# Kernel tuning notes

Hardware: AMD Instinct MI355X
Metric: run time of the kernel (lower is better)

Reference implementation:

```python
import jax, jax.numpy as jnp
import numpy as np

# ---- problem constants (mirror AdjustInstanceArea __init__ args) ----
NUM_NODES = 2_000_000
NUM_MOVABLE = 1_500_000
NUM_FILLER = 400_000
NUM_NETS = 1_500_000
PINS_PER_NET = 4                       # uniform netpin_start = arange(0, P+1, 4)
NUM_PINS = NUM_NETS * PINS_PER_NET
XL, XH, YL, YH = 0.0, 1000.0, 0.0, 1000.0
NBX = NBY = 512
BIN_W = (XH - XL) / NBX
BIN_H = (YH - YL) / NBY
UNIT_H_CAP = 1.5                       # unit horizontal routing capacity
UNIT_V_CAP = 1.5                       # unit vertical routing capacity
MAX_RATE = 2.0                         # max_route_opt_adjust_rate
MIN_RATE = 1.0 / MAX_RATE
EPS = 1e-6


def setup_inputs() -> dict:
    key = jax.random.key(0)
    k = jax.random.split(key, 4)
    x = jax.random.uniform(k[0], (NUM_NODES,), jnp.float32, XL, XH - 4.0)
    y = jax.random.uniform(k[1], (NUM_NODES,), jnp.float32, YL, YH - 4.0)
    pos = jnp.concatenate([x, y])                      # [2*num_nodes], x then y

    # pins clustered around net centers (realistic small net bboxes)
    rng = np.random.default_rng(0)
    centers = rng.uniform(0.0, 1000.0, size=(NUM_NETS, 1, 2)).astype(np.float32)
    jit = rng.uniform(-20.0, 20.0, size=(NUM_NETS, PINS_PER_NET, 2)).astype(np.float32)
    ppos = np.clip(centers + jit, 0.0, 1000.0)         # [nets, pins_per_net, 2], in net order

    # flat_netpin: pin ids grouped by net; pin_pos indexed by pin id
    flat_netpin = rng.permutation(NUM_PINS).astype(np.int32)
    px = np.empty(NUM_PINS, np.float32); py = np.empty(NUM_PINS, np.float32)
    px[flat_netpin] = ppos[..., 0].reshape(-1)
    py[flat_netpin] = ppos[..., 1].reshape(-1)
    pin_pos = jnp.concatenate([jnp.asarray(px), jnp.asarray(py)])  # [2*num_pins]

    pin2net = jnp.asarray(np.repeat(np.arange(NUM_NETS, dtype=np.int32), PINS_PER_NET))

    node_size_x = jax.random.uniform(k[2], (NUM_NODES,), jnp.float32, 1.0, 4.0)
    node_size_y = jax.random.uniform(k[3], (NUM_NODES,), jnp.float32, 1.0, 4.0)
    return {"pos": pos, "pin_pos": pin_pos,
            "node_size_x": node_size_x, "node_size_y": node_size_y,
            "flat_netpin": jnp.asarray(flat_netpin), "pin2net": pin2net}


def _rect_accum(vals, blx, bly, bhx, bhy):
    """Accumulate vals over inclusive bin rectangles via difference map + 2D cumsum."""
    D = jnp.zeros((NBX + 1, NBY + 1), vals.dtype)
    D = D.at[blx, bly].add(vals)
    D = D.at[bhx + 1, bly].add(-vals)
    D = D.at[blx, bhy + 1].add(-vals)
    D = D.at[bhx + 1, bhy + 1].add(vals)
    return jnp.cumsum(jnp.cumsum(D, axis=0), axis=1)[:NBX, :NBY]


def reference(pos, pin_pos, node_size_x, node_size_y, flat_netpin, pin2net):
    # ---- InstanceRouteOptimizationArea: RUDY routing demand per bin ----
    px = pin_pos[:NUM_PINS][flat_netpin].reshape(NUM_NETS, PINS_PER_NET)
    py = pin_pos[NUM_PINS:][flat_netpin].reshape(NUM_NETS, PINS_PER_NET)
    net_xl = jnp.min(px, axis=1); net_xh = jnp.max(px, axis=1)
    net_yl = jnp.min(py, axis=1); net_yh = jnp.max(py, axis=1)
    bw = net_xh - net_xl
    bh = net_yh - net_yl
    barea = jnp.maximum(bw * bh, EPS)
    dens_h = bw / barea                                # horizontal wire density
    dens_v = bh / barea                                # vertical wire density

    blx = jnp.clip(jnp.floor((net_xl - XL) / BIN_W), 0, NBX - 1).astype(jnp.int32)
    bhx = jnp.clip(jnp.floor((net_xh - XL) / BIN_W), 0, NBX - 1).astype(jnp.int32)
    bly = jnp.clip(jnp.floor((net_yl - YL) / BIN_H), 0, NBY - 1).astype(jnp.int32)
    bhy = jnp.clip(jnp.floor((net_yh - YL) / BIN_H), 0, NBY - 1).astype(jnp.int32)

    util_h = _rect_accum(dens_h, blx, bly, bhx, bhy) / UNIT_H_CAP
    util_v = _rect_accum(dens_v, blx, bly, bhx, bhy) / UNIT_V_CAP

    # per-movable-node utilization (gather at node center bin)
    x = pos[:NUM_NODES]; y = pos[NUM_NODES:]
    nsx_m = node_size_x[:NUM_MOVABLE]; nsy_m = node_size_y[:NUM_MOVABLE]
    cx = x[:NUM_MOVABLE] + 0.5 * nsx_m
    cy = y[:NUM_MOVABLE] + 0.5 * nsy_m
    bix = jnp.clip(jnp.floor((cx - XL) / BIN_W), 0, NBX - 1).astype(jnp.int32)
    biy = jnp.clip(jnp.floor((cy - YL) / BIN_H), 0, NBY - 1).astype(jnp.int32)
    util = jnp.maximum(util_h[bix, biy], util_v[bix, biy])
    ratio = jnp.clip(util, MIN_RATE, MAX_RATE)

    area_old = nsx_m * nsy_m
    instance_route_area = area_old * ratio

    # ---- AdjustInstanceArea: rescale under max_total_area budget ----
    filler_area_old = jnp.sum(node_size_x[NUM_NODES - NUM_FILLER:] *
                              node_size_y[NUM_NODES - NUM_FILLER:])
    max_total_area = jnp.sum(area_old) + filler_area_old
    scale = jnp.minimum(1.0, max_total_area / jnp.maximum(jnp.sum(instance_route_area), EPS))
    new_area = instance_route_area * scale
    sr = jnp.sqrt(new_area / jnp.maximum(area_old, EPS))
    nsx_new = nsx_m * sr
    nsy_new = nsy_m * sr

    # keep cell centers fixed while resizing
    x_out = x.at[:NUM_MOVABLE].add(0.5 * (nsx_m - nsx_new))
    y_out = y.at[:NUM_MOVABLE].add(0.5 * (nsy_m - nsy_new))

    # fillers absorb leftover area budget
    fscale = jnp.sqrt(jnp.maximum(max_total_area - jnp.sum(new_area), 0.0) /
                      jnp.maximum(filler_area_old, EPS))
    nsx_out = node_size_x.at[:NUM_MOVABLE].set(nsx_new)
    nsx_out = nsx_out.at[NUM_NODES - NUM_FILLER:].multiply(fscale)
    nsy_out = node_size_y.at[:NUM_MOVABLE].set(nsy_new)
    nsy_out = nsy_out.at[NUM_NODES - NUM_FILLER:].multiply(fscale)

    return jnp.concatenate([x_out, y_out, nsx_out, nsy_out])  # [4*num_nodes]
```

## Files before the change

### kernel.cpp

```cpp
#include <hip/hip_runtime.h>
#include <hip/hip_fp16.h>
#include <math.h>

#define N_NODES   2000000
#define N_MOVABLE 1500000
#define N_FILLER  400000
#define N_NETS    1500000
#define N_PINS    (N_NETS * 4)
#define NB        512
#define NT        16
#define TILE      32
#define NBUCKET   (NT * NT)
#define CAP       10240
#define NSLICE    4
#define NMAPS     NSLICE
#define RED_BLOCKS 1024

#define NQ        24
#define QRNG      250000
#define NXCD      8
#define RPX       3
#define PIN_PER_XCD (QRNG * RPX)
#define P2CHUNK   4096
#define P2CHUNKS  ((PIN_PER_XCD + P2CHUNK - 1) / P2CHUNK)

#define SB_SHIFT  14
#define SB_CAP    16384
#define NSB       ((N_PINS + SB_CAP - 1) / SB_CAP)

__device__ __forceinline__ int bin_idx(float v) {
    float b = floorf(v / 1.953125f);
    b = fminf(fmaxf(b, 0.0f), 511.0f);
    return (int)b;
}

__global__ __launch_bounds__(1024)
void p1_bucketq_kernel(const int* __restrict__ fnp,
                       uint2* __restrict__ qslab,
                       unsigned* __restrict__ g_qptr) {
    __shared__ unsigned hist[NQ];
    __shared__ unsigned hbase[NQ];
    int t = threadIdx.x;
    if (t < NQ) hist[t] = 0;
    __syncthreads();

    int s0 = blockIdx.x * 4096 + t * 4;
    unsigned q[4]; unsigned qb[4]; unsigned rk[4]; bool val[4];
    if (s0 + 3 < N_PINS) {
        int4 f = *reinterpret_cast<const int4*>(fnp + s0);
        q[0] = (unsigned)f.x; q[1] = (unsigned)f.y;
        q[2] = (unsigned)f.z; q[3] = (unsigned)f.w;
        val[0] = val[1] = val[2] = val[3] = true;
    } else {
        #pragma unroll
        for (int j = 0; j < 4; ++j) {
            val[j] = (s0 + j < N_PINS);
            q[j] = val[j] ? (unsigned)fnp[s0 + j] : 0u;
        }
    }
    #pragma unroll
    for (int j = 0; j < 4; ++j) {
        qb[j] = q[j] / (unsigned)QRNG;
        rk[j] = val[j] ? atomicAdd(&hist[qb[j]], 1u) : 0u;
    }
    __syncthreads();
    if (t < NQ) {
        unsigned c = hist[t];
        hbase[t] = c ? atomicAdd(&g_qptr[t], c) : 0u;
    }
    __syncthreads();
    #pragma unroll
    for (int j = 0; j < 4; ++j) {
        if (val[j]) {
            unsigned idx = qb[j] * (unsigned)QRNG + hbase[qb[j]] + rk[j];
            qslab[idx] = make_uint2(q[j], (unsigned)(s0 + j));
        }
    }
}

__global__ __launch_bounds__(1024)
void p2_gather_kernel(const uint2* __restrict__ qslab,
                      const float* __restrict__ pin_pos,
                      uint2* __restrict__ sslab,
                      unsigned* __restrict__ xcd_ctr,
                      unsigned* __restrict__ g_sptr) {
    __shared__ unsigned hist[NSB];
    __shared__ unsigned hbase[NSB];
    __shared__ unsigned sh_c;
    int k = blockIdx.x & (NXCD - 1);
    int t = threadIdx.x;

    for (;;) {
        if (t == 0) sh_c = atomicAdd(&xcd_ctr[k], 1u);
        __syncthreads();
        unsigned c = sh_c;
        __syncthreads();
        if (c >= (unsigned)P2CHUNKS) break;

        for (int i = t; i < NSB; i += 1024) hist[i] = 0;
        __syncthreads();

        uint2 rec[4]; int sb[4]; unsigned rk[4]; bool val[4];
        #pragma unroll
        for (int j = 0; j < 4; ++j) {
            unsigned s = c * P2CHUNK + t + j * 1024;
            val[j] = (s < (unsigned)PIN_PER_XCD);
            sb[j] = 0; rk[j] = 0;
            if (val[j]) {
                unsigned rl = s / (unsigned)QRNG;
                unsigned ridx = s - rl * (unsigned)QRNG;
                unsigned r = (unsigned)k + 8u * rl;
                uint2 qr = qslab[r * (unsigned)QRNG + ridx];
                float x = pin_pos[qr.x];
                float y = pin_pos[qr.x + N_PINS];
                unsigned xq = __float2uint_rn(x * 64.0f);
                unsigned yq = __float2uint_rn(y * 64.0f);
                rec[j] = make_uint2(qr.y, xq | (yq << 16));
                sb[j] = (int)(qr.y >> SB_SHIFT);
                rk[j] = atomicAdd(&hist[sb[j]], 1u);
            }
        }
        __syncthreads();
        for (int i = t; i < NSB; i += 1024) {
            unsigned h = hist[i];
            hbase[i] = h ? atomicAdd(&g_sptr[i], h) : 0u;
        }
        __syncthreads();
        #pragma unroll
        for (int j = 0; j < 4; ++j) {
            if (val[j]) sslab[(size_t)sb[j] * SB_CAP + hbase[sb[j]] + rk[j]] = rec[j];
        }
        __syncthreads();
    }
}

__device__ __forceinline__ uint2 pack_tile_rec(float bw, float bh,
                                               unsigned blx, unsigned bhx,
                                               unsigned bly, unsigned bhy,
                                               int* tb) {
    float barea = fmaxf(bw * bh, 1e-6f);
    float vh = fminf((bw / barea) * (1.0f / 1.5f), 60000.0f);
    float vv = fminf((bh / barea) * (1.0f / 1.5f), 60000.0f);
    *tb = (int)((bly >> 5) * NT + (blx >> 5));
    __half2 h = __float22half2_rn(make_float2(vh, vv));
    uint2 r;
    r.x = *reinterpret_cast<unsigned*>(&h);
    r.y = blx | (bly << 9) | ((bhx + 1 - blx) << 18) | ((bhy + 1 - bly) << 23);
    return r;
}

__global__ __launch_bounds__(512)
void p3_netred_kernel(const uint2* __restrict__ sslab,
                      uint2* __restrict__ tslab,
                      unsigned* __restrict__ g_tptr) {
    __shared__ unsigned mnx[4096], mxx[4096], mny[4096], mxy[4096];
    __shared__ unsigned hist[NBUCKET];
    __shared__ unsigned hbase[NBUCKET];
    int bid = blockIdx.x, t = threadIdx.x;
    int base_slot = bid * SB_CAP;
    int cnt  = min(SB_CAP, N_PINS - base_slot);
    int base_net = bid * (SB_CAP / 4);
    int nets = min(SB_CAP / 4, N_NETS - base_net);

    for (int i = t; i < 4096; i += 512) {
        mnx[i] = 0xFFFFFFFFu; mny[i] = 0xFFFFFFFFu; mxx[i] = 0u; mxy[i] = 0u;
    }
    for (int i = t; i < NBUCKET; i += 512) hist[i] = 0;
    __syncthreads();

    for (int i = t; i < cnt; i += 512) {
        uint2 rc = sslab[(size_t)base_slot + i];
        unsigned nl = (rc.x >> 2) - (unsigned)base_net;
        unsigned xq = rc.y & 0xFFFFu, yq = rc.y >> 16;
        atomicMin(&mnx[nl], xq); atomicMax(&mxx[nl], xq);
        atomicMin(&mny[nl], yq); atomicMax(&mxy[nl], yq);
    }
    __syncthreads();

    uint2 rec[8]; int tb[8]; unsigned rk[8];
    #pragma unroll
    for (int u = 0; u < 8; ++u) {
        int j = t + u * 512;
        tb[u] = -1;
        if (j < nets) {
            unsigned xl = mnx[j], xh = mxx[j], yl = mny[j], yh = mxy[j];
            float bw = (float)(xh - xl) * 0.015625f;
            float bh = (float)(yh - yl) * 0.015625f;
            unsigned blx = min(xl / 125u, 511u), bhx = min(xh / 125u, 511u);
            unsigned bly = min(yl / 125u, 511u), bhy = min(yh / 125u, 511u);
            rec[u] = pack_tile_rec(bw, bh, blx, bhx, bly, bhy, &tb[u]);
            rk[u] = atomicAdd(&hist[tb[u]], 1u);
        }
    }
    __syncthreads();
    if (t < NBUCKET) {
        unsigned h = hist[t];
        hbase[t] = h ? atomicAdd(&g_tptr[t], h) : 0u;
    }
    __syncthreads();
    #pragma unroll
    for (int u = 0; u < 8; ++u) {
        if (tb[u] >= 0) tslab[(size_t)tb[u] * CAP + hbase[tb[u]] + rk[u]] = rec[u];
    }
}

__global__ void pack_kernel(const float* __restrict__ pin_pos,
                            float2* __restrict__ pp) {
    int i = blockIdx.x * blockDim.x + threadIdx.x;
    if (i >= N_PINS / 4) return;
    float4 a = reinterpret_cast<const float4*>(pin_pos)[i];
    float4 b = reinterpret_cast<const float4*>(pin_pos + N_PINS)[i];
    float4* o = reinterpret_cast<float4*>(pp + 4 * (size_t)i);
    o[0] = make_float4(a.x, b.x, a.y, b.y);
    o[1] = make_float4(a.z, b.z, a.w, b.w);
}

template <bool PACKED>
__device__ __forceinline__ uint2 make_rec_f(const float* __restrict__ pin_pos,
                                            const float2* __restrict__ pp,
                                            int4 fp, int* tb) {
    float2 p0, p1, p2, p3;
    if (PACKED) {
        p0 = pp[fp.x]; p1 = pp[fp.y]; p2 = pp[fp.z]; p3 = pp[fp.w];
    } else {
        p0 = make_float2(pin_pos[fp.x], pin_pos[N_PINS + fp.x]);
        p1 = make_float2(pin_pos[fp.y], pin_pos[N_PINS + fp.y]);
        p2 = make_float2(pin_pos[fp.z], pin_pos[N_PINS + fp.z]);
        p3 = make_float2(pin_pos[fp.w], pin_pos[N_PINS + fp.w]);
    }
    float xl = fminf(fminf(p0.x, p1.x), fminf(p2.x, p3.x));
    float xh = fmaxf(fmaxf(p0.x, p1.x), fmaxf(p2.x, p3.x));
    float yl = fminf(fminf(p0.y, p1.y), fminf(p2.y, p3.y));
    float yh = fmaxf(fmaxf(p0.y, p1.y), fmaxf(p2.y, p3.y));
    unsigned blx = bin_idx(xl), bhx = bin_idx(xh);
    unsigned bly = bin_idx(yl), bhy = bin_idx(yh);
    return pack_tile_rec(xh - xl, yh - yl, blx, bhx, bly, bhy, tb);
}

template <bool PACKED>
__global__ __launch_bounds__(1024)
void gather_bin_kernel(const float* __restrict__ pin_pos,
                       const float2* __restrict__ pp,
                       const int* __restrict__ fnp,
                       uint2* __restrict__ slab,
                       unsigned* __restrict__ g_ptr) {
    __shared__ unsigned hist[NBUCKET];
    __shared__ unsigned hbase[NBUCKET];
    int t = threadIdx.x;
    if (t < NBUCKET) hist[t] = 0;
    __syncthreads();

    int n0 = blockIdx.x * 4096 + t;
    bool v[4]; int4 fp[4]; uint2 r[4]; int b[4]; unsigned rk[4];
    #pragma unroll
    for (int k = 0; k < 4; ++k) {
        int n = n0 + k * 1024;
        v[k] = (n < N_NETS);
        fp[k] = v[k] ? *reinterpret_cast<const int4*>(fnp + 4 * (size_t)n)
                     : make_int4(0, 0, 0, 0);
    }
    #pragma unroll
    for (int k = 0; k < 4; ++k) {
        b[k] = 0;
        if (v[k]) r[k] = make_rec_f<PACKED>(pin_pos, pp, fp[k], &b[k]);
    }
    #pragma unroll
    for (int k = 0; k < 4; ++k) rk[k] = v[k] ? atomicAdd(&hist[b[k]], 1u) : 0u;
    __syncthreads();
    if (t < NBUCKET) {
        unsigned c = hist[t];
        hbase[t] = c ? atomicAdd(&g_ptr[t], c) : 0u;
    }
    __syncthreads();
    #pragma unroll
    for (int k = 0; k < 4; ++k) {
        if (v[k]) {
            unsigned s = hbase[b[k]] + rk[k];
            if (s < CAP) slab[(size_t)b[k] * CAP + s] = r[k];
        }
    }
}

__device__ __forceinline__ void rec_process(uint2 r, int x0, int y0,
                                            float2* acc) {
    float2 v = __half22float2(*reinterpret_cast<const __half2*>(&r.x));
    unsigned g = r.y;
    int ax0 = (int)(g & 511u);
    int ay0 = (int)((g >> 9) & 511u);
    int ax1 = ax0 + (int)((g >> 18) & 31u);
    int ay1 = ay0 + (int)((g >> 23) & 31u);
    int X0 = ax0 - x0, Y0 = ay0 - y0;
    int X1 = ax1 - x0, Y1 = ay1 - y0;
    bool iX0 = (unsigned)X0 < TILE, iX1 = (unsigned)X1 < TILE;
    bool iY0 = (unsigned)Y0 < TILE, iY1 = (unsigned)Y1 < TILE;
    if (iX0 && iY0) { atomicAdd(&acc[X0 * TILE + Y0].x,  v.x); atomicAdd(&acc[X0 * TILE + Y0].y,  v.y); }
    if (iX1 && iY0) { atomicAdd(&acc[X1 * TILE + Y0].x, -v.x); atomicAdd(&acc[X1 * TILE + Y0].y, -v.y); }
    if (iX0 && iY1) { atomicAdd(&acc[X0 * TILE + Y1].x, -v.x); atomicAdd(&acc[X0 * TILE + Y1].y, -v.y); }
    if (iX1 && iY1) { atomicAdd(&acc[X1 * TILE + Y1].x,  v.x); atomicAdd(&acc[X1 * TILE + Y1].y,  v.y); }
}

__global__ __launch_bounds__(256)
void accum_kernel(const uint2* __restrict__ slab,
                  const unsigned* __restrict__ g_cnt,
                  float2* __restrict__ Dp) {
    __shared__ float2 acc[TILE * TILE];
    int wg = blockIdx.x;
    int sl = wg & (NSLICE - 1), tile = wg >> 2;
    int tx = tile & (NT - 1), ty = tile >> 4;
    int tid = threadIdx.x;

    for (int i = tid; i < TILE * TILE; i += 256) acc[i] = make_float2(0.f, 0.f);
    __syncthreads();

    int x0 = tx * TILE, y0 = ty * TILE;
    #pragma unroll
    for (int dy = -1; dy <= 0; ++dy) {
        int sy = ty + dy; if (sy < 0) continue;
        #pragma unroll
        for (int dx = -1; dx <= 0; ++dx) {
            int sx = tx + dx; if (sx < 0) continue;
            int sb = sy * NT + sx;
            unsigned cnt = min(g_cnt[sb], (unsigned)CAP);
            unsigned lo = (cnt * (unsigned)sl) >> 2;
            unsigned hi = (cnt * (unsigned)(sl + 1)) >> 2;
            const uint2* recs = slab + (size_t)sb * CAP;
            unsigned i = lo + tid;
            for (; i + 768 < hi; i += 1024) {
                uint2 r0 = recs[i];
                uint2 r1 = recs[i + 256];
                uint2 r2 = recs[i + 512];
                uint2 r3 = recs[i + 768];
                rec_process(r0, x0, y0, acc);
                rec_process(r1, x0, y0, acc);
                rec_process(r2, x0, y0, acc);
                rec_process(r3, x0, y0, acc);
            }
            for (; i < hi; i += 256) rec_process(recs[i], x0, y0, acc);
        }
    }
    __syncthreads();

    float2* D = Dp + (size_t)sl * NB * NB;
    for (int i = tid; i < TILE * TILE; i += 256) {
        int X = i >> 5, Y = i & 31;
        D[(size_t)(x0 + X) * NB + (y0 + Y)] = acc[i];
    }
}

__global__ __launch_bounds__(512)
void scanA_kernel(const float2* __restrict__ Dp, float2* __restrict__ S) {
    __shared__ float2 s[NB];
    int x = blockIdx.x, t = threadIdx.x;
    float2 a = make_float2(0.f, 0.f);
    #pragma unroll
    for (int m = 0; m < NMAPS; ++m) {
        float2 v = Dp[(size_t)m * NB * NB + (size_t)x * NB + t];
        a.x += v.x; a.y += v.y;
    }
    s[t] = a;
    __syncthreads();
    for (int off = 1; off < NB; off <<= 1) {
        float2 u = s[t];
        if (t >= off) { float2 w = s[t - off]; u.x += w.x; u.y += w.y; }
        __syncthreads();
        s[t] = u;
        __syncthreads();
    }
    S[(size_t)x * NB + t] = s[t];
}

__global__ __launch_bounds__(512)
void scanB_kernel(float2* __restrict__ S) {
    __shared__ float2 s[NB];
    int y = blockIdx.x, t = threadIdx.x;
    s[t] = S[(size_t)t * NB + y];
    __syncthreads();
    for (int off = 1; off < NB; off <<= 1) {
        float2 u = s[t];
        if (t >= off) { float2 w = s[t - off]; u.x += w.x; u.y += w.y; }
        __syncthreads();
        s[t] = u;
        __syncthreads();
    }
    S[(size_t)t * NB + y] = s[t];
}

__global__ __launch_bounds__(256)
void reduce_kernel(const float* __restrict__ pos,
                   const float* __restrict__ nsx,
                   const float* __restrict__ nsy,
                   const float2* __restrict__ S,
                   double* __restrict__ partials) {
    const int MQ = N_MOVABLE / 4;
    const int TQ = MQ + N_FILLER / 4;
    double a_old = 0.0, a_route = 0.0, a_fill = 0.0;
    int stride = gridDim.x * blockDim.x;
    for (int q = blockIdx.x * blockDim.x + threadIdx.x; q < TQ; q += stride) {
        if (q < MQ) {
            int i = 4 * q;
            float4 x4  = *reinterpret_cast<const float4*>(pos + i);
            float4 y4  = *reinterpret_cast<const float4*>(pos + N_NODES + i);
            float4 sx4 = *reinterpret_cast<const float4*>(nsx + i);
            float4 sy4 = *reinterpret_cast<const float4*>(nsy + i);
            float xs[4] = {x4.x, x4.y, x4.z, x4.w};
            float ys[4] = {y4.x, y4.y, y4.z, y4.w};
            float sxs[4] = {sx4.x, sx4.y, sx4.z, sx4.w};
            float sys[4] = {sy4.x, sy4.y, sy4.z, sy4.w};
            #pragma unroll
            for (int k = 0; k < 4; ++k) {
                int bx = bin_idx(xs[k] + 0.5f * sxs[k]);
                int by = bin_idx(ys[k] + 0.5f * sys[k]);
                float2 u2 = S[(size_t)bx * NB + by];
                float ratio = fminf(fmaxf(fmaxf(u2.x, u2.y), 0.5f), 2.0f);
                float area = sxs[k] * sys[k];
                a_old += (double)area;
                a_route += (double)(area * ratio);
            }
        } else {
            int j = (N_NODES - N_FILLER) + 4 * (q - MQ);
            float4 sx4 = *reinterpret_cast<const float4*>(nsx + j);
            float4 sy4 = *reinterpret_cast<const float4*>(nsy + j);
            a_fill += (double)(sx4.x * sy4.x + sx4.y * sy4.y +
                               sx4.z * sy4.z + sx4.w * sy4.w);
        }
    }
    for (int off = 32; off > 0; off >>= 1) {
        a_old   += __shfl_down(a_old, off);
        a_route += __shfl_down(a_route, off);
        a_fill  += __shfl_down(a_fill, off);
    }
    __shared__ double sd[4][3];
    int wid = threadIdx.x >> 6, lane = threadIdx.x & 63;
    if (lane == 0) { sd[wid][0] = a_old; sd[wid][1] = a_route; sd[wid][2] = a_fill; }
    __syncthreads();
    if (threadIdx.x == 0) {
        double s0 = 0, s1 = 0, s2 = 0;
        for (int w = 0; w < 4; ++w) { s0 += sd[w][0]; s1 += sd[w][1]; s2 += sd[w][2]; }
        partials[blockIdx.x * 3 + 0] = s0;
        partials[blockIdx.x * 3 + 1] = s1;
        partials[blockIdx.x * 3 + 2] = s2;
    }
}

__global__ __launch_bounds__(256)
void finish_kernel(const double* __restrict__ partials,
                   double* __restrict__ sums) {
    int t = threadIdx.x;
    double s0 = 0, s1 = 0, s2 = 0;
    for (int r = t; r < RED_BLOCKS; r += 256) {
        s0 += partials[r * 3 + 0];
        s1 += partials[r * 3 + 1];
        s2 += partials[r * 3 + 2];
    }
    for (int off = 32; off > 0; off >>= 1) {
        s0 += __shfl_down(s0, off);
        s1 += __shfl_down(s1, off);
        s2 += __shfl_down(s2, off);
    }
    __shared__ double sd[4][3];
    int wid = t >> 6, lane = t & 63;
    if (lane == 0) { sd[wid][0] = s0; sd[wid][1] = s1; sd[wid][2] = s2; }
    __syncthreads();
    if (t == 0) {
        double a = 0, b = 0, c = 0;
        for (int w = 0; w < 4; ++w) { a += sd[w][0]; b += sd[w][1]; c += sd[w][2]; }
        sums[0] = a; sums[1] = b; sums[2] = c;
    }
}

__global__ __launch_bounds__(256)
void final_kernel(const float* __restrict__ pos,
                  const float* __restrict__ nsx,
                  const float* __restrict__ nsy,
                  const float2* __restrict__ S,
                  const double* __restrict__ sums,
                  float* __restrict__ out) {
    double sum_area  = sums[0];
    double sum_route = sums[1];
    double fill_old  = sums[2];
    double max_total = sum_area + fill_old;

    float scale = fminf(1.0f, (float)(max_total / fmax(sum_route, 1e-6)));
    float sum_new = (float)(scale * (float)sum_route);
    float fscale = sqrtf(fmaxf((float)max_total - sum_new, 0.0f) /
                         fmaxf((float)fill_old, 1e-6f));

    int q = blockIdx.x * blockDim.x + threadIdx.x;
    if (q >= N_NODES / 4) return;
    int i = 4 * q;

    float4 x4  = *reinterpret_cast<const float4*>(pos + i);
    float4 y4  = *reinterpret_cast<const float4*>(pos + N_NODES + i);
    float4 sx4 = *reinterpret_cast<const float4*>(nsx + i);
    float4 sy4 = *reinterpret_cast<const float4*>(nsy + i);

    float xs[4] = {x4.x, x4.y, x4.z, x4.w};
    float ys[4] = {y4.x, y4.y, y4.z, y4.w};
    float sxs[4] = {sx4.x, sx4.y, sx4.z, sx4.w};
    float sys[4] = {sy4.x, sy4.y, sy4.z, sy4.w};

    if (i < N_MOVABLE) {
        #pragma unroll
        for (int k = 0; k < 4; ++k) {
            int bx = bin_idx(xs[k] + 0.5f * sxs[k]);
            int by = bin_idx(ys[k] + 0.5f * sys[k]);
            float2 u2 = S[(size_t)bx * NB + by];
            float ratio = fminf(fmaxf(fmaxf(u2.x, u2.y), 0.5f), 2.0f);
            float area = sxs[k] * sys[k];
            float new_area = area * ratio * scale;
            float sr = sqrtf(new_area / fmaxf(area, 1e-6f));
            float sx_new = sxs[k] * sr, sy_new = sys[k] * sr;
            xs[k] = xs[k] + 0.5f * (sxs[k] - sx_new);
            ys[k] = ys[k] + 0.5f * (sys[k] - sy_new);
            sxs[k] = sx_new; sys[k] = sy_new;
        }
    } else if (i >= N_NODES - N_FILLER) {
        #pragma unroll
        for (int k = 0; k < 4; ++k) { sxs[k] *= fscale; sys[k] *= fscale; }
    }

    *reinterpret_cast<float4*>(out + i)               = make_float4(xs[0], xs[1], xs[2], xs[3]);
    *reinterpret_cast<float4*>(out + N_NODES + i)     = make_float4(ys[0], ys[1], ys[2], ys[3]);
    *reinterpret_cast<float4*>(out + 2 * N_NODES + i) = make_float4(sxs[0], sxs[1], sxs[2], sxs[3]);
    *reinterpret_cast<float4*>(out + 3 * N_NODES + i) = make_float4(sys[0], sys[1], sys[2], sys[3]);
}

extern "C" void kernel_launch(void* const* d_in, const int* in_sizes, int n_in,
                              void* d_out, int out_size, void* d_ws, size_t ws_size,
                              hipStream_t stream) {
    const float* pos         = (const float*)d_in[0];
    const float* pin_pos     = (const float*)d_in[1];
    const float* nsx         = (const float*)d_in[2];
    const float* nsy         = (const float*)d_in[3];
    const int*   flat_netpin = (const int*)d_in[4];
    float* out = (float*)d_out;

    const size_t qslab_b = (size_t)N_PINS * sizeof(uint2);
    const size_t sslab_b = (size_t)NSB * SB_CAP * sizeof(uint2);
    const size_t tslab_b = (size_t)NBUCKET * CAP * sizeof(uint2);
    const size_t ctr_b   = 4096;
    const size_t dp_b    = (size_t)NMAPS * NB * NB * sizeof(float2);
    const size_t s_b     = (size_t)NB * NB * sizeof(float2);
    const size_t part_b  = (size_t)RED_BLOCKS * 3 * sizeof(double);
    const size_t pp_b    = (size_t)N_PINS * sizeof(float2);

    const size_t need_new = qslab_b + sslab_b + tslab_b + ctr_b;
    const size_t need_r8  = pp_b + tslab_b + ctr_b;

    char* base = (char*)d_ws;
    int tier = (ws_size >= need_new) ? 0 : (ws_size >= need_r8) ? 1 : 2;

    uint2* tslab; unsigned* ctrs; float2* Dp; float2* S;
    double* partials; double* sums;

    if (tier == 0) {
        uint2* qslab = (uint2*)base;
        uint2* sslab = (uint2*)(base + qslab_b);
        tslab        = (uint2*)(base + qslab_b + sslab_b);
        ctrs         = (unsigned*)(base + qslab_b + sslab_b + tslab_b);
        Dp       = (float2*)base;
        S        = (float2*)(base + dp_b);
        partials = (double*)(base + dp_b + s_b);
        sums     = (double*)(base + dp_b + s_b + part_b);

        unsigned* g_qptr  = ctrs;
        unsigned* xcd_ctr = ctrs + 32;
        unsigned* g_sptr  = ctrs + 64;
        unsigned* g_tptr  = ctrs + 448;

        hipMemsetAsync(ctrs, 0, ctr_b, stream);
        p1_bucketq_kernel<<<(N_PINS + 4095) / 4096, 1024, 0, stream>>>(
            flat_netpin, qslab, g_qptr);
        p2_gather_kernel<<<P2CHUNKS * NXCD, 1024, 0, stream>>>(
            qslab, pin_pos, sslab, xcd_ctr, g_sptr);
        p3_netred_kernel<<<NSB, 512, 0, stream>>>(sslab, tslab, g_tptr);

        accum_kernel <<<NBUCKET * NSLICE, 256, 0, stream>>>(tslab, g_tptr, Dp);
    } else if (tier == 1) {
        float2* pp = (float2*)base;
        tslab      = (uint2*)(base + pp_b);
        ctrs       = (unsigned*)(base + pp_b + tslab_b);
        Dp       = (float2*)base;
        S        = (float2*)(base + dp_b);
        partials = (double*)(base + dp_b + s_b);
        sums     = (double*)(base + dp_b + s_b + part_b);
        unsigned* g_tptr = ctrs + 448;

        hipMemsetAsync(ctrs, 0, ctr_b, stream);
        pack_kernel<<<(N_PINS / 4 + 255) / 256, 256, 0, stream>>>(pin_pos, pp);
        gather_bin_kernel<true><<<(N_NETS + 4095) / 4096, 1024, 0, stream>>>(
            pin_pos, pp, flat_netpin, tslab, g_tptr);
        accum_kernel <<<NBUCKET * NSLICE, 256, 0, stream>>>(tslab, g_tptr, Dp);
    } else {
        tslab = (uint2*)base;
        Dp    = (float2*)(base + tslab_b);
        S     = (float2*)(base + tslab_b + dp_b);
        partials = (double*)(base + tslab_b + dp_b + s_b);
        sums     = (double*)(base + tslab_b + dp_b + s_b + part_b);
        ctrs     = (unsigned*)(base + tslab_b + dp_b + s_b + part_b + 64);
        unsigned* g_tptr = ctrs + 448;

        hipMemsetAsync(ctrs, 0, ctr_b, stream);
        gather_bin_kernel<false><<<(N_NETS + 4095) / 4096, 1024, 0, stream>>>(
            pin_pos, nullptr, flat_netpin, tslab, g_tptr);
        accum_kernel <<<NBUCKET * NSLICE, 256, 0, stream>>>(tslab, ctrs + 448, Dp);
    }

    scanA_kernel <<<NB, 512, 0, stream>>>(Dp, S);
    scanB_kernel <<<NB, 512, 0, stream>>>(S);
    reduce_kernel<<<RED_BLOCKS, 256, 0, stream>>>(pos, nsx, nsy, S, partials);
    finish_kernel<<<1, 256, 0, stream>>>(partials, sums);
    final_kernel <<<(N_NODES / 4 + 255) / 256, 256, 0, stream>>>(pos, nsx, nsy, S, sums, out);
}
```

Measured before the change: 249.9 us.

## Replace sorted-slab net reduction with direct scatter to slot-indexed pin array

The gather kernel now writes each quantized pin coordinate straight into a dense array indexed by flat slot, instead of building per-block histograms and appending to super-bucket slabs. The net kernel then reads four packed pins per net as one uint4 and computes the bbox in registers, with no shared-memory atomics. This removes the sslab bucketing pass, the per-chunk dynamic work counter and the 4-array atomic min/max reduction. In exchange the gather does scattered 4-byte writes, and a CAP bound check is added on tslab writes.

```diff
diff --git a/kernel.cpp b/kernel.cpp
--- a/kernel.cpp
+++ b/kernel.cpp
@@ -24,10 +24,6 @@
 #define P2CHUNK   4096
 #define P2CHUNKS  ((PIN_PER_XCD + P2CHUNK - 1) / P2CHUNK)
 
-#define SB_SHIFT  14
-#define SB_CAP    16384
-#define NSB       ((N_PINS + SB_CAP - 1) / SB_CAP)
-
 __device__ __forceinline__ int bin_idx(float v) {
     float b = floorf(v / 1.953125f);
     b = fminf(fmaxf(b, 0.0f), 511.0f);
@@ -81,56 +77,23 @@
 __global__ __launch_bounds__(1024)
 void p2_gather_kernel(const uint2* __restrict__ qslab,
                       const float* __restrict__ pin_pos,
-                      uint2* __restrict__ sslab,
-                      unsigned* __restrict__ xcd_ctr,
-                      unsigned* __restrict__ g_sptr) {
-    __shared__ unsigned hist[NSB];
-    __shared__ unsigned hbase[NSB];
-    __shared__ unsigned sh_c;
-    int k = blockIdx.x & (NXCD - 1);
-    int t = threadIdx.x;
-
-    for (;;) {
-        if (t == 0) sh_c = atomicAdd(&xcd_ctr[k], 1u);
-        __syncthreads();
-        unsigned c = sh_c;
-        __syncthreads();
-        if (c >= (unsigned)P2CHUNKS) break;
-
-        for (int i = t; i < NSB; i += 1024) hist[i] = 0;
-        __syncthreads();
-
-        uint2 rec[4]; int sb[4]; unsigned rk[4]; bool val[4];
-        #pragma unroll
-        for (int j = 0; j < 4; ++j) {
-            unsigned s = c * P2CHUNK + t + j * 1024;
-            val[j] = (s < (unsigned)PIN_PER_XCD);
-            sb[j] = 0; rk[j] = 0;
-            if (val[j]) {
-                unsigned rl = s / (unsigned)QRNG;
-                unsigned ridx = s - rl * (unsigned)QRNG;
-                unsigned r = (unsigned)k + 8u * rl;
-                uint2 qr = qslab[r * (unsigned)QRNG + ridx];
-                float x = pin_pos[qr.x];
-                float y = pin_pos[qr.x + N_PINS];
-                unsigned xq = __float2uint_rn(x * 64.0f);
-                unsigned yq = __float2uint_rn(y * 64.0f);
-                rec[j] = make_uint2(qr.y, xq | (yq << 16));
-                sb[j] = (int)(qr.y >> SB_SHIFT);
-                rk[j] = atomicAdd(&hist[sb[j]], 1u);
-            }
-        }
-        __syncthreads();
-        for (int i = t; i < NSB; i += 1024) {
-            unsigned h = hist[i];
-            hbase[i] = h ? atomicAdd(&g_sptr[i], h) : 0u;
-        }
-        __syncthreads();
-        #pragma unroll
-        for (int j = 0; j < 4; ++j) {
-            if (val[j]) sslab[(size_t)sb[j] * SB_CAP + hbase[sb[j]] + rk[j]] = rec[j];
-        }
-        __syncthreads();
+                      unsigned* __restrict__ sxy) {
+    unsigned k = blockIdx.x & (NXCD - 1);
+    unsigned c = blockIdx.x >> 3;
+    unsigned t = threadIdx.x;
+    #pragma unroll
+    for (int j = 0; j < 4; ++j) {
+        unsigned s = c * (unsigned)P2CHUNK + t + (unsigned)j * 1024u;
+        if (s < (unsigned)PIN_PER_XCD) {
+            unsigned rl = s / (unsigned)QRNG;
+            unsigned ridx = s - rl * (unsigned)QRNG;
+            uint2 qr = qslab[(k + 8u * rl) * (unsigned)QRNG + ridx];
+            float x = pin_pos[qr.x];
+            float y = pin_pos[qr.x + N_PINS];
+            unsigned xq = __float2uint_rn(x * 64.0f);
+            unsigned yq = __float2uint_rn(y * 64.0f);
+            sxy[qr.y] = xq | (yq << 16);
+        }
     }
 }
 
@@ -149,41 +112,32 @@
     return r;
 }
 
-__global__ __launch_bounds__(512)
-void p3_netred_kernel(const uint2* __restrict__ sslab,
+__global__ __launch_bounds__(1024)
+void p3_netrec_kernel(const unsigned* __restrict__ sxy,
                       uint2* __restrict__ tslab,
                       unsigned* __restrict__ g_tptr) {
-    __shared__ unsigned mnx[4096], mxx[4096], mny[4096], mxy[4096];
     __shared__ unsigned hist[NBUCKET];
     __shared__ unsigned hbase[NBUCKET];
-    int bid = blockIdx.x, t = threadIdx.x;
-    int base_slot = bid * SB_CAP;
-    int cnt  = min(SB_CAP, N_PINS - base_slot);
-    int base_net = bid * (SB_CAP / 4);
-    int nets = min(SB_CAP / 4, N_NETS - base_net);
-
-    for (int i = t; i < 4096; i += 512) {
-        mnx[i] = 0xFFFFFFFFu; mny[i] = 0xFFFFFFFFu; mxx[i] = 0u; mxy[i] = 0u;
-    }
-    for (int i = t; i < NBUCKET; i += 512) hist[i] = 0;
-    __syncthreads();
-
-    for (int i = t; i < cnt; i += 512) {
-        uint2 rc = sslab[(size_t)base_slot + i];
-        unsigned nl = (rc.x >> 2) - (unsigned)base_net;
-        unsigned xq = rc.y & 0xFFFFu, yq = rc.y >> 16;
-        atomicMin(&mnx[nl], xq); atomicMax(&mxx[nl], xq);
-        atomicMin(&mny[nl], yq); atomicMax(&mxy[nl], yq);
-    }
-    __syncthreads();
-
-    uint2 rec[8]; int tb[8]; unsigned rk[8];
-    #pragma unroll
-    for (int u = 0; u < 8; ++u) {
-        int j = t + u * 512;
+    int t = threadIdx.x;
+    if (t < NBUCKET) hist[t] = 0;
+    __syncthreads();
+
+    int n0 = blockIdx.x * 4096 + t;
+    uint2 rec[4]; int tb[4]; unsigned rk[4];
+    #pragma unroll
+    for (int u = 0; u < 4; ++u) {
+        int n = n0 + u * 1024;
         tb[u] = -1;
-        if (j < nets) {
-            unsigned xl = mnx[j], xh = mxx[j], yl = mny[j], yh = mxy[j];
+        if (n < N_NETS) {
+            uint4 v = *reinterpret_cast<const uint4*>(sxy + 4 * (size_t)n);
+            unsigned x0 = v.x & 0xffffu, y0 = v.x >> 16;
+            unsigned x1 = v.y & 0xffffu, y1 = v.y >> 16;
+            unsigned x2 = v.z & 0xffffu, y2 = v.z >> 16;
+            unsigned x3 = v.w & 0xffffu, y3 = v.w >> 16;
+            unsigned xl = min(min(x0, x1), min(x2, x3));
+            unsigned xh = max(max(x0, x1), max(x2, x3));
+            unsigned yl = min(min(y0, y1), min(y2, y3));
+            unsigned yh = max(max(y0, y1), max(y2, y3));
             float bw = (float)(xh - xl) * 0.015625f;
             float bh = (float)(yh - yl) * 0.015625f;
             unsigned blx = min(xl / 125u, 511u), bhx = min(xh / 125u, 511u);
@@ -194,13 +148,16 @@
     }
     __syncthreads();
     if (t < NBUCKET) {
-        unsigned h = hist[t];
-        hbase[t] = h ? atomicAdd(&g_tptr[t], h) : 0u;
-    }
-    __syncthreads();
-    #pragma unroll
-    for (int u = 0; u < 8; ++u) {
-        if (tb[u] >= 0) tslab[(size_t)tb[u] * CAP + hbase[tb[u]] + rk[u]] = rec[u];
+        unsigned c = hist[t];
+        hbase[t] = c ? atomicAdd(&g_tptr[t], c) : 0u;
+    }
+    __syncthreads();
+    #pragma unroll
+    for (int u = 0; u < 4; ++u) {
+        if (tb[u] >= 0) {
+            unsigned s = hbase[tb[u]] + rk[u];
+            if (s < CAP) tslab[(size_t)tb[u] * CAP + s] = rec[u];
+        }
     }
 }
 
@@ -536,7 +493,7 @@
     float* out = (float*)d_out;
 
     const size_t qslab_b = (size_t)N_PINS * sizeof(uint2);
-    const size_t sslab_b = (size_t)NSB * SB_CAP * sizeof(uint2);
+    const size_t sxy_b   = (size_t)N_PINS * sizeof(unsigned);
     const size_t tslab_b = (size_t)NBUCKET * CAP * sizeof(uint2);
     const size_t ctr_b   = 4096;
     const size_t dp_b    = (size_t)NMAPS * NB * NB * sizeof(float2);
@@ -544,7 +501,7 @@
     const size_t part_b  = (size_t)RED_BLOCKS * 3 * sizeof(double);
     const size_t pp_b    = (size_t)N_PINS * sizeof(float2);
 
-    const size_t need_new = qslab_b + sslab_b + tslab_b + ctr_b;
+    const size_t need_new = qslab_b + sxy_b + tslab_b + ctr_b;
     const size_t need_r8  = pp_b + tslab_b + ctr_b;
 
     char* base = (char*)d_ws;
@@ -554,27 +511,25 @@
     double* partials; double* sums;
 
     if (tier == 0) {
-        uint2* qslab = (uint2*)base;
-        uint2* sslab = (uint2*)(base + qslab_b);
-        tslab        = (uint2*)(base + qslab_b + sslab_b);
-        ctrs         = (unsigned*)(base + qslab_b + sslab_b + tslab_b);
+        uint2*    qslab = (uint2*)base;
+        unsigned* sxy   = (unsigned*)(base + qslab_b);
+        tslab           = (uint2*)(base + qslab_b + sxy_b);
+        ctrs            = (unsigned*)(base + qslab_b + sxy_b + tslab_b);
         Dp       = (float2*)base;
         S        = (float2*)(base + dp_b);
         partials = (double*)(base + dp_b + s_b);
         sums     = (double*)(base + dp_b + s_b + part_b);
 
-        unsigned* g_qptr  = ctrs;
-        unsigned* xcd_ctr = ctrs + 32;
-        unsigned* g_sptr  = ctrs + 64;
-        unsigned* g_tptr  = ctrs + 448;
+        unsigned* g_qptr = ctrs;
+        unsigned* g_tptr = ctrs + 448;
 
         hipMemsetAsync(ctrs, 0, ctr_b, stream);
         p1_bucketq_kernel<<<(N_PINS + 4095) / 4096, 1024, 0, stream>>>(
             flat_netpin, qslab, g_qptr);
         p2_gather_kernel<<<P2CHUNKS * NXCD, 1024, 0, stream>>>(
-            qslab, pin_pos, sslab, xcd_ctr, g_sptr);
-        p3_netred_kernel<<<NSB, 512, 0, stream>>>(sslab, tslab, g_tptr);
-
+            qslab, pin_pos, sxy);
+        p3_netrec_kernel<<<(N_NETS + 4095) / 4096, 1024, 0, stream>>>(
+            sxy, tslab, g_tptr);
         accum_kernel <<<NBUCKET * NSLICE, 256, 0, stream>>>(tslab, g_tptr, Dp);
     } else if (tier == 1) {
         float2* pp = (float2*)base;
@@ -603,7 +558,7 @@
         hipMemsetAsync(ctrs, 0, ctr_b, stream);
         gather_bin_kernel<false><<<(N_NETS + 4095) / 4096, 1024, 0, stream>>>(
             pin_pos, nullptr, flat_netpin, tslab, g_tptr);
-        accum_kernel <<<NBUCKET * NSLICE, 256, 0, stream>>>(tslab, ctrs + 448, Dp);
+        accum_kernel <<<NBUCKET * NSLICE, 256, 0, stream>>>(tslab, g_tptr, Dp);
     }
 
     scanA_kernel <<<NB, 512, 0, stream>>>(Dp, S);
```

After: 262.8 us. 5.2% more time.
